# Optimization experiments

Measured on AMD Instinct MI355X. Metric: run time of the kernel, lower is better.

Reference implementation:

```python
import jax, jax.numpy as jnp
import numpy as np

B, S, D, H = 2, 2048, 1024, 16
HD = D // H  # head_dim = 64
SCALE = HD ** -0.5


def setup_inputs() -> dict:
    key = jax.random.key(0)
    k1, k2, k3 = jax.random.split(key, 3)
    src = jax.random.normal(k1, (B, S, D), dtype=jnp.float32)
    w_qkv = jax.random.normal(k2, (D, 3 * D), dtype=jnp.float32) * (D ** -0.5)
    b_qkv = jax.random.normal(k3, (3 * D,), dtype=jnp.float32) * 0.02
    return {"src": src, "w_qkv": w_qkv, "b_qkv": b_qkv}


def reference(src, w_qkv, b_qkv):
    # qkv projection: [B,S,3D]
    qkv = src @ w_qkv + b_qkv
    q, k, v = jnp.split(qkv, 3, axis=-1)
    # [B,S,D] -> [B,H,S,HD]
    def heads(x):
        return x.reshape(B, S, H, HD).transpose(0, 2, 1, 3)
    q, k, v = heads(q), heads(k), heads(v)
    # scaled dot-product attention (note: original scales AFTER q@k.T)
    attn = jnp.einsum('bhqd,bhkd->bhqk', q, k) * SCALE
    attn = jax.nn.softmax(attn, axis=-1)
    out = jnp.einsum('bhqk,bhkd->bhqd', attn, v)  # [B,H,S,HD]
    return out.transpose(0, 2, 1, 3).reshape(B, S, D)
```

## Files before the change

### kernel.cpp

```cpp
#include <hip/hip_runtime.h>
#include <hip/hip_bf16.h>

typedef short short8 __attribute__((ext_vector_type(8)));
typedef float f32x4 __attribute__((ext_vector_type(4)));
typedef float f32x16 __attribute__((ext_vector_type(16)));
typedef __hip_bfloat16 bf16;


__device__ __forceinline__ void glds16(const void* g, void* l) {
  __builtin_amdgcn_global_load_lds((const __attribute__((address_space(1))) unsigned int*)g,
                                   (__attribute__((address_space(3))) unsigned int*)l, 16, 0, 0);
}

__global__ __launch_bounds__(256) void cvt_src_kernel(const float4* __restrict__ in,
                                                      bf16* __restrict__ out, int n4) {
  int i = blockIdx.x * 256 + threadIdx.x;
  if (i >= n4) return;
  float4 v = in[i];
  union { bf16 h[4]; uint2 u; } pk;
  pk.h[0] = __float2bfloat16(v.x);
  pk.h[1] = __float2bfloat16(v.y);
  pk.h[2] = __float2bfloat16(v.z);
  pk.h[3] = __float2bfloat16(v.w);
  *(uint2*)(out + (size_t)i * 4) = pk.u;
}

__global__ __launch_bounds__(256) void transpose_w_kernel(const float* __restrict__ w,
                                                          bf16* __restrict__ wt) {
  __shared__ float tile[32][33];
  int x0 = blockIdx.x * 32;
  int y0 = blockIdx.y * 32;
  int tx = threadIdx.x & 31, ty = threadIdx.x >> 5;
#pragma unroll
  for (int i = 0; i < 4; i++) {
    int y = ty + i * 8;
    tile[y][tx] = w[(size_t)(y0 + y) * 3072 + x0 + tx];
  }
  __syncthreads();
#pragma unroll
  for (int i = 0; i < 4; i++) {
    int y = ty + i * 8;
    wt[(size_t)(x0 + y) * 1024 + y0 + tx] = __float2bfloat16(tile[tx][y]);
  }
}

__global__ __launch_bounds__(256) void qkv_gemm_kernel(
    const bf16* __restrict__ A, const bf16* __restrict__ Bt,
    const float* __restrict__ bias,
    bf16* __restrict__ q_ws, bf16* __restrict__ k_ws, bf16* __restrict__ vt_ws) {
  __shared__ alignas(16) char AB[32768];
  const int tid = threadIdx.x;
  const int lane = tid & 63, wid = tid >> 6;
  const int lr = lane & 15, lg = lane >> 4;
  const int wm = wid >> 1, wn = wid & 1;
  const int m0 = blockIdx.x * 128, n0 = blockIdx.y * 128;

  const f32x4 z4 = {0.f, 0.f, 0.f, 0.f};
  f32x4 acc[4][4];
#pragma unroll
  for (int m = 0; m < 4; m++)
#pragma unroll
    for (int n = 0; n < 4; n++) acc[m][n] = z4;

  const int srow = lane >> 3;
  const int sseg = (lane & 7) ^ srow;
  const char* Ag = (const char*)A + (size_t)(m0 + wid * 32 + srow) * 2048 + sseg * 16;
  const char* Bg = (const char*)Bt + (size_t)(n0 + wid * 32 + srow) * 2048 + sseg * 16;
  char* Al = AB + wid * 4096;
  char* Bl = AB + 16384 + wid * 4096;
  const int xora = (lr & 7) << 4;

  for (int kt = 0; kt < 16; kt++) {
    __syncthreads();
#pragma unroll
    for (int c = 0; c < 4; c++) {
      glds16(Ag + (size_t)kt * 128 + c * 16384, Al + c * 1024);
      glds16(Bg + (size_t)kt * 128 + c * 16384, Bl + c * 1024);
    }
    asm volatile("s_waitcnt vmcnt(0)" ::: "memory");
    __syncthreads();
#pragma unroll
    for (int g = 0; g < 2; g++) {
      short8 af[4], bfr[4];
#pragma unroll
      for (int m = 0; m < 4; m++)
        af[m] = *(const short8*)(AB + (wm * 64 + m * 16 + lr) * 128 +
                                 ((g * 64 + lg * 16) ^ xora));
#pragma unroll
      for (int n = 0; n < 4; n++)
        bfr[n] = *(const short8*)(AB + 16384 + (wn * 64 + n * 16 + lr) * 128 +
                                  ((g * 64 + lg * 16) ^ xora));
#pragma unroll
      for (int m = 0; m < 4; m++)
#pragma unroll
        for (int n = 0; n < 4; n++)
          acc[m][n] = __builtin_amdgcn_mfma_f32_16x16x32_bf16(af[m], bfr[n], acc[m][n], 0, 0, 0);
    }
  }

  const int which = n0 >> 10;
#pragma unroll
  for (int m = 0; m < 4; m++) {
    int row = m0 + wm * 64 + m * 16 + lg * 4;
    int b = row >> 11;
    int ss0 = row & 2047;
#pragma unroll
    for (int n = 0; n < 4; n++) {
      int col = n0 + wn * 64 + n * 16 + lr;
      int d = col & 1023;
      int h = d >> 6, hd = d & 63;
      size_t bh = (size_t)(b * 16 + h);
      float bv = bias[col];
      if (which == 2) {
        union { bf16 h4[4]; uint2 u; } pk;
#pragma unroll
        for (int r = 0; r < 4; r++) pk.h4[r] = __float2bfloat16(acc[m][n][r] + bv);
        *(uint2*)&vt_ws[(bh * 64 + hd) * 2048 + ss0] = pk.u;
      } else {
        bf16* dst = (which == 0) ? q_ws : k_ws;
#pragma unroll
        for (int r = 0; r < 4; r++)
          dst[(bh * 2048 + (ss0 + r)) * 64 + hd] = __float2bfloat16(acc[m][n][r] + bv);
      }
    }
  }
}

__global__ __launch_bounds__(512) void attn2_kernel(
    const bf16* __restrict__ q_ws, const bf16* __restrict__ k_ws,
    const bf16* __restrict__ vt_ws, float* __restrict__ out) {
  __shared__ alignas(16) char smem[65536];
  const int tid = threadIdx.x;
  const int lane = tid & 63, wid = tid >> 6;
  const int lq = lane & 31, hi = lane >> 5;
  const int hi16 = hi * 16;
  const int xorv = (lq & 7) << 4;
  const float scale_l2e = 0.125f * 1.44269504088896f;

  const int f = blockIdx.x;
  const int bh = (f & 7) * 4 + ((f >> 3) & 3);
  const int qb = f >> 5;
  const int b = bh >> 4, h = bh & 15;
  const int q0 = qb * 256 + wid * 32;

  short8 qf[4];
  {
    const bf16* qrow = q_ws + ((size_t)bh * 2048 + q0 + lq) * 64;
#pragma unroll
    for (int s = 0; s < 4; s++) qf[s] = *(const short8*)(qrow + s * 16 + hi * 8);
  }

  const int seg = (lane & 7) ^ (lane >> 3);
  const char* kgl = (const char*)k_ws + (size_t)bh * 2048 * 128 +
                    (size_t)(wid * 8 + (lane >> 3)) * 128 + seg * 16;
  const char* vgl = (const char*)vt_ws + (size_t)bh * 64 * 4096 +
                    (size_t)(wid * 8 + (lane >> 3)) * 4096 + seg * 16;

  f32x16 o0, o1;
#pragma unroll
  for (int r = 0; r < 16; r++) { o0[r] = 0.f; o1[r] = 0.f; }
  float m = -1e30f, l = 0.f;

#pragma unroll
  for (int p = 0; p < 3; p++) {
    glds16(kgl + (size_t)p * 8192, smem + p * 8192 + wid * 1024);
    glds16(vgl + (size_t)p * 128, smem + 32768 + p * 8192 + wid * 1024);
  }
  asm volatile("s_waitcnt vmcnt(4)" ::: "memory");
  __builtin_amdgcn_s_barrier();

  for (int kt = 0; kt < 32; ++kt) {
    const int buf = kt & 3;
    if (kt + 3 < 32) {
      glds16(kgl + (size_t)(kt + 3) * 8192, smem + ((kt + 3) & 3) * 8192 + wid * 1024);
      glds16(vgl + (size_t)(kt + 3) * 128, smem + 32768 + ((kt + 3) & 3) * 8192 + wid * 1024);
    }
    const int curK = buf * 8192;
    const int curV = 32768 + buf * 8192;

    f32x16 s0, s1;
#pragma unroll
    for (int r = 0; r < 16; r++) { s0[r] = 0.f; s1[r] = 0.f; }
#pragma unroll
    for (int s = 0; s < 4; s++) {
      const int doff = (s * 32 + hi16) ^ xorv;
      short8 k0 = *(const short8*)(smem + curK + lq * 128 + doff);
      short8 k1 = *(const short8*)(smem + curK + 4096 + lq * 128 + doff);
      __builtin_amdgcn_s_setprio(1);
      s0 = __builtin_amdgcn_mfma_f32_32x32x16_bf16(k0, qf[s], s0, 0, 0, 0);
      s1 = __builtin_amdgcn_mfma_f32_32x32x16_bf16(k1, qf[s], s1, 0, 0, 0);
      __builtin_amdgcn_s_setprio(0);
    }

    float mx[8];
#pragma unroll
    for (int r = 0; r < 16; r++) { s0[r] *= scale_l2e; s1[r] *= scale_l2e; }
#pragma unroll
    for (int i = 0; i < 8; i++) mx[i] = fmaxf(fmaxf(s0[i], s0[i + 8]), fmaxf(s1[i], s1[i + 8]));
#pragma unroll
    for (int i = 0; i < 4; i++) mx[i] = fmaxf(mx[i], mx[i + 4]);
    float pm = fmaxf(fmaxf(mx[0], mx[1]), fmaxf(mx[2], mx[3]));
    pm = fmaxf(pm, __shfl_xor(pm, 32));
    if (pm > m + 8.f) {
      float rs = __builtin_amdgcn_exp2f(m - pm);
      m = pm; l *= rs;
#pragma unroll
      for (int r = 0; r < 16; r++) { o0[r] *= rs; o1[r] *= rs; }
    }
    float sum[8];
#pragma unroll
    for (int r = 0; r < 16; r++) {
      s0[r] = __builtin_amdgcn_exp2f(s0[r] - m);
      s1[r] = __builtin_amdgcn_exp2f(s1[r] - m);
    }
#pragma unroll
    for (int i = 0; i < 8; i++) sum[i] = (s0[i] + s0[i + 8]) + (s1[i] + s1[i + 8]);
#pragma unroll
    for (int i = 0; i < 4; i++) sum[i] += sum[i + 4];
    float ps = (sum[0] + sum[1]) + (sum[2] + sum[3]);
    ps += __shfl_xor(ps, 32);
    l += ps;

#pragma unroll
    for (int kb = 0; kb < 2; kb++) {
      uint w[8], t[8];
#pragma unroll
      for (int i = 0; i < 8; i++) {
        union { bf16 h2[2]; uint u; } pk;
        float plo = kb ? s1[2 * i] : s0[2 * i];
        float phi = kb ? s1[2 * i + 1] : s0[2 * i + 1];
        pk.h2[0] = __float2bfloat16(plo);
        pk.h2[1] = __float2bfloat16(phi);
        w[i] = pk.u;
      }
#pragma unroll
      for (int i = 0; i < 8; i++) t[i] = (uint)__shfl_xor((int)w[i], 32);
      union { uint u[4]; short8 s; } ua, ub;
      ua.u[0] = hi ? t[2] : w[0];
      ua.u[1] = hi ? t[3] : w[1];
      ua.u[2] = hi ? w[2] : t[0];
      ua.u[3] = hi ? w[3] : t[1];
      ub.u[0] = hi ? t[6] : w[4];
      ub.u[1] = hi ? t[7] : w[5];
      ub.u[2] = hi ? w[6] : t[4];
      ub.u[3] = hi ? w[7] : t[5];
#pragma unroll
      for (int s = 0; s < 2; s++) {
        short8 pa = s ? ub.s : ua.s;
        const int koff = (kb * 64 + s * 32 + hi16) ^ xorv;
        short8 v0 = *(const short8*)(smem + curV + lq * 128 + koff);
        short8 v1 = *(const short8*)(smem + curV + 4096 + lq * 128 + koff);
        __builtin_amdgcn_s_setprio(1);
        o0 = __builtin_amdgcn_mfma_f32_32x32x16_bf16(v0, pa, o0, 0, 0, 0);
        o1 = __builtin_amdgcn_mfma_f32_32x32x16_bf16(v1, pa, o1, 0, 0, 0);
        __builtin_amdgcn_s_setprio(0);
      }
    }

    if (kt < 29)       asm volatile("s_waitcnt vmcnt(4)" ::: "memory");
    else if (kt == 29) asm volatile("s_waitcnt vmcnt(2)" ::: "memory");
    else if (kt == 30) asm volatile("s_waitcnt vmcnt(0)" ::: "memory");
    if (kt < 31) __builtin_amdgcn_s_barrier();
  }
  __syncthreads();

  float* ep = (float*)(smem) + wid * 1024;
  const float invl = 1.f / l;
  const int eq = lane >> 1, eds = lane & 1;
  float* obase = out + ((size_t)b * 2048 + qb * 256 + wid * 32 + eq) * 1024 +
                 h * 64 + eds * 16;
#pragma unroll
  for (int db = 0; db < 2; db++) {
#pragma unroll
    for (int r = 0; r < 16; r++) {
      int d = (r & 3) + 8 * (r >> 2) + 4 * hi;
      float v = (db ? o1[r] : o0[r]) * invl;
      ep[lq * 32 + ((d + lq) & 31)] = v;
    }
#pragma unroll
    for (int c = 0; c < 4; c++) {
      float4 t;
      t.x = ep[eq * 32 + ((eds * 16 + 4 * c + 0 + eq) & 31)];
      t.y = ep[eq * 32 + ((eds * 16 + 4 * c + 1 + eq) & 31)];
      t.z = ep[eq * 32 + ((eds * 16 + 4 * c + 2 + eq) & 31)];
      t.w = ep[eq * 32 + ((eds * 16 + 4 * c + 3 + eq) & 31)];
      *(float4*)(obase + db * 32 + 4 * c) = t;
    }
  }
}

extern "C" void kernel_launch(void* const* d_in, const int* in_sizes, int n_in,
                              void* d_out, int out_size, void* d_ws, size_t ws_size,
                              hipStream_t stream) {
  (void)in_sizes; (void)n_in; (void)out_size; (void)ws_size;
  const float* src  = (const float*)d_in[0];
  const float* w    = (const float*)d_in[1];
  const float* bias = (const float*)d_in[2];
  float* out = (float*)d_out;

  char* ws = (char*)d_ws;
  bf16* src_bf = (bf16*)ws;
  bf16* wt_bf  = (bf16*)(ws + 8388608);
  bf16* q_ws   = (bf16*)(ws + 8388608 + 6291456);
  bf16* k_ws   = q_ws + 4194304;
  bf16* vt_ws  = k_ws + 4194304;

  cvt_src_kernel<<<4096, 256, 0, stream>>>((const float4*)src, src_bf, 1048576);
  transpose_w_kernel<<<dim3(96, 32), 256, 0, stream>>>(w, wt_bf);
  qkv_gemm_kernel<<<dim3(32, 24), 256, 0, stream>>>(src_bf, wt_bf, bias, q_ws, k_ws, vt_ws);
  attn2_kernel<<<256, 512, 0, stream>>>(q_ws, k_ws, vt_ws, out);
}
```

Measured before the change: 107.7 us.

## Split attention KV range across two blocks and merge partials in new kernel

Attention grid doubles from 256 to 512 blocks. Each block processes half of the key/value sequence and writes an unnormalized partial output plus its running max and sum to workspace. A new merge kernel combines the two halves with log-sum-exp weights. The intent is to fill the MI355X's 256 CUs with more than one wave of blocks, at the cost of an extra launch and extra global traffic. The score scaling is also folded into an fma inside exp2, and the max is scaled once after reduction.

```diff
diff --git a/kernel.cpp b/kernel.cpp
--- a/kernel.cpp
+++ b/kernel.cpp
@@ -128,7 +128,7 @@
 
 __global__ __launch_bounds__(512) void attn2_kernel(
     const bf16* __restrict__ q_ws, const bf16* __restrict__ k_ws,
-    const bf16* __restrict__ vt_ws, float* __restrict__ out) {
+    const bf16* __restrict__ vt_ws, float* __restrict__ po, float* __restrict__ ml) {
   __shared__ alignas(16) char smem[65536];
   const int tid = threadIdx.x;
   const int lane = tid & 63, wid = tid >> 6;
@@ -138,9 +138,10 @@
   const float scale_l2e = 0.125f * 1.44269504088896f;
 
   const int f = blockIdx.x;
-  const int bh = (f & 7) * 4 + ((f >> 3) & 3);
-  const int qb = f >> 5;
-  const int b = bh >> 4, h = bh & 15;
+  const int ks = f & 1;
+  const int g = f >> 1;
+  const int bh = (g & 7) * 4 + ((g >> 3) & 3);
+  const int qb = g >> 5;
   const int q0 = qb * 256 + wid * 32;
 
   short8 qf[4];
@@ -151,9 +152,9 @@
   }
 
   const int seg = (lane & 7) ^ (lane >> 3);
-  const char* kgl = (const char*)k_ws + (size_t)bh * 2048 * 128 +
+  const char* kgl = (const char*)k_ws + (size_t)bh * 2048 * 128 + (size_t)ks * 16 * 8192 +
                     (size_t)(wid * 8 + (lane >> 3)) * 128 + seg * 16;
-  const char* vgl = (const char*)vt_ws + (size_t)bh * 64 * 4096 +
+  const char* vgl = (const char*)vt_ws + (size_t)bh * 64 * 4096 + ks * 2048 +
                     (size_t)(wid * 8 + (lane >> 3)) * 4096 + seg * 16;
 
   f32x16 o0, o1;
@@ -169,9 +170,9 @@
   asm volatile("s_waitcnt vmcnt(4)" ::: "memory");
   __builtin_amdgcn_s_barrier();
 
-  for (int kt = 0; kt < 32; ++kt) {
+  for (int kt = 0; kt < 16; ++kt) {
     const int buf = kt & 3;
-    if (kt + 3 < 32) {
+    if (kt + 3 < 16) {
       glds16(kgl + (size_t)(kt + 3) * 8192, smem + ((kt + 3) & 3) * 8192 + wid * 1024);
       glds16(vgl + (size_t)(kt + 3) * 128, smem + 32768 + ((kt + 3) & 3) * 8192 + wid * 1024);
     }
@@ -194,13 +195,12 @@
 
     float mx[8];
 #pragma unroll
-    for (int r = 0; r < 16; r++) { s0[r] *= scale_l2e; s1[r] *= scale_l2e; }
-#pragma unroll
     for (int i = 0; i < 8; i++) mx[i] = fmaxf(fmaxf(s0[i], s0[i + 8]), fmaxf(s1[i], s1[i + 8]));
 #pragma unroll
     for (int i = 0; i < 4; i++) mx[i] = fmaxf(mx[i], mx[i + 4]);
     float pm = fmaxf(fmaxf(mx[0], mx[1]), fmaxf(mx[2], mx[3]));
     pm = fmaxf(pm, __shfl_xor(pm, 32));
+    pm *= scale_l2e;
     if (pm > m + 8.f) {
       float rs = __builtin_amdgcn_exp2f(m - pm);
       m = pm; l *= rs;
@@ -210,8 +210,8 @@
     float sum[8];
 #pragma unroll
     for (int r = 0; r < 16; r++) {
-      s0[r] = __builtin_amdgcn_exp2f(s0[r] - m);
-      s1[r] = __builtin_amdgcn_exp2f(s1[r] - m);
+      s0[r] = __builtin_amdgcn_exp2f(__builtin_fmaf(s0[r], scale_l2e, -m));
+      s1[r] = __builtin_amdgcn_exp2f(__builtin_fmaf(s1[r], scale_l2e, -m));
     }
 #pragma unroll
     for (int i = 0; i < 8; i++) sum[i] = (s0[i] + s0[i + 8]) + (s1[i] + s1[i + 8]);
@@ -257,24 +257,26 @@
       }
     }
 
-    if (kt < 29)       asm volatile("s_waitcnt vmcnt(4)" ::: "memory");
-    else if (kt == 29) asm volatile("s_waitcnt vmcnt(2)" ::: "memory");
-    else if (kt == 30) asm volatile("s_waitcnt vmcnt(0)" ::: "memory");
-    if (kt < 31) __builtin_amdgcn_s_barrier();
+    if (kt < 13)       asm volatile("s_waitcnt vmcnt(4)" ::: "memory");
+    else if (kt == 13) asm volatile("s_waitcnt vmcnt(2)" ::: "memory");
+    else if (kt == 14) asm volatile("s_waitcnt vmcnt(0)" ::: "memory");
+    if (kt < 15) __builtin_amdgcn_s_barrier();
   }
   __syncthreads();
 
+  if (hi == 0) {
+    float2 v = {m, l};
+    *(float2*)&ml[((size_t)(ks * 32 + bh) * 2048 + q0 + lq) * 2] = v;
+  }
   float* ep = (float*)(smem) + wid * 1024;
-  const float invl = 1.f / l;
   const int eq = lane >> 1, eds = lane & 1;
-  float* obase = out + ((size_t)b * 2048 + qb * 256 + wid * 32 + eq) * 1024 +
-                 h * 64 + eds * 16;
+  float* pobase = po + ((size_t)(ks * 32 + bh) * 2048 + q0 + eq) * 64 + eds * 16;
 #pragma unroll
   for (int db = 0; db < 2; db++) {
 #pragma unroll
     for (int r = 0; r < 16; r++) {
       int d = (r & 3) + 8 * (r >> 2) + 4 * hi;
-      float v = (db ? o1[r] : o0[r]) * invl;
+      float v = (db ? o1[r] : o0[r]);
       ep[lq * 32 + ((d + lq) & 31)] = v;
     }
 #pragma unroll
@@ -284,9 +286,36 @@
       t.y = ep[eq * 32 + ((eds * 16 + 4 * c + 1 + eq) & 31)];
       t.z = ep[eq * 32 + ((eds * 16 + 4 * c + 2 + eq) & 31)];
       t.w = ep[eq * 32 + ((eds * 16 + 4 * c + 3 + eq) & 31)];
-      *(float4*)(obase + db * 32 + 4 * c) = t;
-    }
-  }
+      *(float4*)(pobase + db * 32 + 4 * c) = t;
+    }
+  }
+}
+
+__global__ __launch_bounds__(256) void merge_kernel(const float* __restrict__ po,
+                                                    const float* __restrict__ ml,
+                                                    float* __restrict__ out) {
+  int i = blockIdx.x * 256 + threadIdx.x;
+  int c4 = i & 255;
+  int bs = i >> 8;
+  int h = c4 >> 4, hd4 = c4 & 15;
+  int b = bs >> 11, s = bs & 2047;
+  size_t row0 = (size_t)(b * 16 + h) * 2048 + s;
+  size_t row1 = (size_t)(32 + b * 16 + h) * 2048 + s;
+  float2 ml0 = *(const float2*)&ml[row0 * 2];
+  float2 ml1 = *(const float2*)&ml[row1 * 2];
+  float M = fmaxf(ml0.x, ml1.x);
+  float w0 = __builtin_amdgcn_exp2f(ml0.x - M);
+  float w1 = __builtin_amdgcn_exp2f(ml1.x - M);
+  float inv = 1.f / (ml0.y * w0 + ml1.y * w1);
+  w0 *= inv; w1 *= inv;
+  float4 a = *(const float4*)&po[row0 * 64 + hd4 * 4];
+  float4 c = *(const float4*)&po[row1 * 64 + hd4 * 4];
+  float4 r;
+  r.x = a.x * w0 + c.x * w1;
+  r.y = a.y * w0 + c.y * w1;
+  r.z = a.z * w0 + c.z * w1;
+  r.w = a.w * w0 + c.w * w1;
+  *(float4*)&out[(size_t)bs * 1024 + c4 * 4] = r;
 }
 
 extern "C" void kernel_launch(void* const* d_in, const int* in_sizes, int n_in,
@@ -299,14 +328,17 @@
   float* out = (float*)d_out;
 
   char* ws = (char*)d_ws;
+  float* po = (float*)ws;
+  float* ml = (float*)(ws + 33554432);
   bf16* src_bf = (bf16*)ws;
   bf16* wt_bf  = (bf16*)(ws + 8388608);
-  bf16* q_ws   = (bf16*)(ws + 8388608 + 6291456);
+  bf16* q_ws   = (bf16*)(ws + 34603008);
   bf16* k_ws   = q_ws + 4194304;
   bf16* vt_ws  = k_ws + 4194304;
 
   cvt_src_kernel<<<4096, 256, 0, stream>>>((const float4*)src, src_bf, 1048576);
   transpose_w_kernel<<<dim3(96, 32), 256, 0, stream>>>(w, wt_bf);
   qkv_gemm_kernel<<<dim3(32, 24), 256, 0, stream>>>(src_bf, wt_bf, bias, q_ws, k_ws, vt_ws);
-  attn2_kernel<<<256, 512, 0, stream>>>(q_ws, k_ws, vt_ws, out);
-}
+  attn2_kernel<<<512, 512, 0, stream>>>(q_ws, k_ws, vt_ws, po, ml);
+  merge_kernel<<<4096, 256, 0, stream>>>(po, ml, out);
+}
```

After: 116.2 us. 7.9% more time.

## Process 128-key tiles with double buffering and split PV accumulators in attention

Applied to the files above, without the earlier changes.

The attention kernel now processes 128 keys per iteration instead of 64. It uses two shared-memory buffers in place of four, and a new swizzle layout for the V tile. That halves the number of barriers and waits, gives more independent MFMAs per tile, and uses two accumulator sets per output half so dependent MFMA chains are shorter. The scale is folded into an FMA inside exp2, and the lane-exchange shuffles are cut from 8 to 4 per key block. In exchange, register pressure rises and the prefetch is only one tile ahead, waiting on vmcnt(0) every iteration, which may expose load latency.

```diff
diff --git a/kernel.cpp b/kernel.cpp
--- a/kernel.cpp
+++ b/kernel.cpp
@@ -10,6 +10,13 @@
 __device__ __forceinline__ void glds16(const void* g, void* l) {
   __builtin_amdgcn_global_load_lds((const __attribute__((address_space(1))) unsigned int*)g,
                                    (__attribute__((address_space(3))) unsigned int*)l, 16, 0, 0);
+}
+
+__device__ __forceinline__ uint pk2(float a, float b) {
+  union { bf16 h2[2]; uint u; } pk;
+  pk.h2[0] = __float2bfloat16(a);
+  pk.h2[1] = __float2bfloat16(b);
+  return pk.u;
 }
 
 __global__ __launch_bounds__(256) void cvt_src_kernel(const float4* __restrict__ in,
@@ -126,7 +133,7 @@
   }
 }
 
-__global__ __launch_bounds__(512) void attn2_kernel(
+__global__ __launch_bounds__(512) void attn3_kernel(
     const bf16* __restrict__ q_ws, const bf16* __restrict__ k_ws,
     const bf16* __restrict__ vt_ws, float* __restrict__ out) {
   __shared__ alignas(16) char smem[65536];
@@ -150,120 +157,142 @@
     for (int s = 0; s < 4; s++) qf[s] = *(const short8*)(qrow + s * 16 + hi * 8);
   }
 
-  const int seg = (lane & 7) ^ (lane >> 3);
-  const char* kgl = (const char*)k_ws + (size_t)bh * 2048 * 128 +
-                    (size_t)(wid * 8 + (lane >> 3)) * 128 + seg * 16;
-  const char* vgl = (const char*)vt_ws + (size_t)bh * 64 * 4096 +
-                    (size_t)(wid * 8 + (lane >> 3)) * 4096 + seg * 16;
-
-  f32x16 o0, o1;
-#pragma unroll
-  for (int r = 0; r < 16; r++) { o0[r] = 0.f; o1[r] = 0.f; }
+  const int l8 = lane >> 3;
+  const int segk = (lane & 7) ^ l8;
+  const char* kgl = (const char*)k_ws + (size_t)bh * 262144 +
+                    (size_t)(wid * 16 + l8) * 128 + segk * 16;
+  const int l16 = lane >> 4;
+  const int d0v = (wid * 2 + 0) * 4 + l16;
+  const int d1v = (wid * 2 + 1) * 4 + l16;
+  const char* vg0 = (const char*)vt_ws + (size_t)bh * 262144 + (size_t)d0v * 4096 +
+                    (((lane & 15) ^ (d0v & 15)) << 4);
+  const char* vg1 = (const char*)vt_ws + (size_t)bh * 262144 + (size_t)d1v * 4096 +
+                    (((lane & 15) ^ (d1v & 15)) << 4);
+
+  f32x16 o0a, o0b, o1a, o1b;
+#pragma unroll
+  for (int r = 0; r < 16; r++) { o0a[r] = 0.f; o0b[r] = 0.f; o1a[r] = 0.f; o1b[r] = 0.f; }
   float m = -1e30f, l = 0.f;
 
-#pragma unroll
-  for (int p = 0; p < 3; p++) {
-    glds16(kgl + (size_t)p * 8192, smem + p * 8192 + wid * 1024);
-    glds16(vgl + (size_t)p * 128, smem + 32768 + p * 8192 + wid * 1024);
-  }
-  asm volatile("s_waitcnt vmcnt(4)" ::: "memory");
+  glds16(kgl, smem + wid * 2048);
+  glds16(kgl + 1024, smem + wid * 2048 + 1024);
+  glds16(vg0, smem + 32768 + wid * 2048);
+  glds16(vg1, smem + 32768 + wid * 2048 + 1024);
+  asm volatile("s_waitcnt vmcnt(0)" ::: "memory");
   __builtin_amdgcn_s_barrier();
 
-  for (int kt = 0; kt < 32; ++kt) {
-    const int buf = kt & 3;
-    if (kt + 3 < 32) {
-      glds16(kgl + (size_t)(kt + 3) * 8192, smem + ((kt + 3) & 3) * 8192 + wid * 1024);
-      glds16(vgl + (size_t)(kt + 3) * 128, smem + 32768 + ((kt + 3) & 3) * 8192 + wid * 1024);
-    }
-    const int curK = buf * 8192;
-    const int curV = 32768 + buf * 8192;
-
-    f32x16 s0, s1;
-#pragma unroll
-    for (int r = 0; r < 16; r++) { s0[r] = 0.f; s1[r] = 0.f; }
-#pragma unroll
-    for (int s = 0; s < 4; s++) {
-      const int doff = (s * 32 + hi16) ^ xorv;
-      short8 k0 = *(const short8*)(smem + curK + lq * 128 + doff);
-      short8 k1 = *(const short8*)(smem + curK + 4096 + lq * 128 + doff);
+  for (int kt = 0; kt < 16; ++kt) {
+    const int kb_off = (kt & 1) * 16384;
+    const int vb_off = 32768 + (kt & 1) * 16384;
+    if (kt + 1 < 16) {
+      const int nb = ((kt + 1) & 1) * 16384;
+      glds16(kgl + (size_t)(kt + 1) * 16384, smem + nb + wid * 2048);
+      glds16(kgl + (size_t)(kt + 1) * 16384 + 1024, smem + nb + wid * 2048 + 1024);
+      glds16(vg0 + (size_t)(kt + 1) * 256, smem + 32768 + nb + wid * 2048);
+      glds16(vg1 + (size_t)(kt + 1) * 256, smem + 32768 + nb + wid * 2048 + 1024);
+    }
+
+    f32x16 s0, s1, s2, s3;
+#pragma unroll
+    for (int r = 0; r < 16; r++) { s0[r] = 0.f; s1[r] = 0.f; s2[r] = 0.f; s3[r] = 0.f; }
+#pragma unroll
+    for (int st = 0; st < 4; st++) {
+      const int doff = (st * 32 + hi16) ^ xorv;
+      short8 ka = *(const short8*)(smem + kb_off + lq * 128 + doff);
+      short8 kb = *(const short8*)(smem + kb_off + (lq + 32) * 128 + doff);
+      short8 kc = *(const short8*)(smem + kb_off + (lq + 64) * 128 + doff);
+      short8 kd = *(const short8*)(smem + kb_off + (lq + 96) * 128 + doff);
       __builtin_amdgcn_s_setprio(1);
-      s0 = __builtin_amdgcn_mfma_f32_32x32x16_bf16(k0, qf[s], s0, 0, 0, 0);
-      s1 = __builtin_amdgcn_mfma_f32_32x32x16_bf16(k1, qf[s], s1, 0, 0, 0);
+      s0 = __builtin_amdgcn_mfma_f32_32x32x16_bf16(ka, qf[st], s0, 0, 0, 0);
+      s1 = __builtin_amdgcn_mfma_f32_32x32x16_bf16(kb, qf[st], s1, 0, 0, 0);
+      s2 = __builtin_amdgcn_mfma_f32_32x32x16_bf16(kc, qf[st], s2, 0, 0, 0);
+      s3 = __builtin_amdgcn_mfma_f32_32x32x16_bf16(kd, qf[st], s3, 0, 0, 0);
       __builtin_amdgcn_s_setprio(0);
     }
 
-    float mx[8];
-#pragma unroll
-    for (int r = 0; r < 16; r++) { s0[r] *= scale_l2e; s1[r] *= scale_l2e; }
-#pragma unroll
-    for (int i = 0; i < 8; i++) mx[i] = fmaxf(fmaxf(s0[i], s0[i + 8]), fmaxf(s1[i], s1[i + 8]));
+    float mx[16];
+#pragma unroll
+    for (int i = 0; i < 16; i++)
+      mx[i] = fmaxf(fmaxf(s0[i], s1[i]), fmaxf(s2[i], s3[i]));
+#pragma unroll
+    for (int i = 0; i < 8; i++) mx[i] = fmaxf(mx[i], mx[i + 8]);
 #pragma unroll
     for (int i = 0; i < 4; i++) mx[i] = fmaxf(mx[i], mx[i + 4]);
     float pm = fmaxf(fmaxf(mx[0], mx[1]), fmaxf(mx[2], mx[3]));
     pm = fmaxf(pm, __shfl_xor(pm, 32));
+    pm *= scale_l2e;
     if (pm > m + 8.f) {
       float rs = __builtin_amdgcn_exp2f(m - pm);
       m = pm; l *= rs;
 #pragma unroll
-      for (int r = 0; r < 16; r++) { o0[r] *= rs; o1[r] *= rs; }
-    }
-    float sum[8];
+      for (int r = 0; r < 16; r++) {
+        o0a[r] *= rs; o0b[r] *= rs; o1a[r] *= rs; o1b[r] *= rs;
+      }
+    }
 #pragma unroll
     for (int r = 0; r < 16; r++) {
-      s0[r] = __builtin_amdgcn_exp2f(s0[r] - m);
-      s1[r] = __builtin_amdgcn_exp2f(s1[r] - m);
-    }
-#pragma unroll
-    for (int i = 0; i < 8; i++) sum[i] = (s0[i] + s0[i + 8]) + (s1[i] + s1[i + 8]);
-#pragma unroll
-    for (int i = 0; i < 4; i++) sum[i] += sum[i + 4];
-    float ps = (sum[0] + sum[1]) + (sum[2] + sum[3]);
-    ps += __shfl_xor(ps, 32);
-    l += ps;
-
-#pragma unroll
-    for (int kb = 0; kb < 2; kb++) {
-      uint w[8], t[8];
-#pragma unroll
-      for (int i = 0; i < 8; i++) {
-        union { bf16 h2[2]; uint u; } pk;
-        float plo = kb ? s1[2 * i] : s0[2 * i];
-        float phi = kb ? s1[2 * i + 1] : s0[2 * i + 1];
-        pk.h2[0] = __float2bfloat16(plo);
-        pk.h2[1] = __float2bfloat16(phi);
-        w[i] = pk.u;
-      }
-#pragma unroll
-      for (int i = 0; i < 8; i++) t[i] = (uint)__shfl_xor((int)w[i], 32);
-      union { uint u[4]; short8 s; } ua, ub;
-      ua.u[0] = hi ? t[2] : w[0];
-      ua.u[1] = hi ? t[3] : w[1];
-      ua.u[2] = hi ? w[2] : t[0];
-      ua.u[3] = hi ? w[3] : t[1];
-      ub.u[0] = hi ? t[6] : w[4];
-      ub.u[1] = hi ? t[7] : w[5];
-      ub.u[2] = hi ? w[6] : t[4];
-      ub.u[3] = hi ? w[7] : t[5];
-#pragma unroll
-      for (int s = 0; s < 2; s++) {
-        short8 pa = s ? ub.s : ua.s;
-        const int koff = (kb * 64 + s * 32 + hi16) ^ xorv;
-        short8 v0 = *(const short8*)(smem + curV + lq * 128 + koff);
-        short8 v1 = *(const short8*)(smem + curV + 4096 + lq * 128 + koff);
-        __builtin_amdgcn_s_setprio(1);
-        o0 = __builtin_amdgcn_mfma_f32_32x32x16_bf16(v0, pa, o0, 0, 0, 0);
-        o1 = __builtin_amdgcn_mfma_f32_32x32x16_bf16(v1, pa, o1, 0, 0, 0);
-        __builtin_amdgcn_s_setprio(0);
-      }
-    }
-
-    if (kt < 29)       asm volatile("s_waitcnt vmcnt(4)" ::: "memory");
-    else if (kt == 29) asm volatile("s_waitcnt vmcnt(2)" ::: "memory");
-    else if (kt == 30) asm volatile("s_waitcnt vmcnt(0)" ::: "memory");
-    if (kt < 31) __builtin_amdgcn_s_barrier();
+      s0[r] = __builtin_amdgcn_exp2f(__builtin_fmaf(s0[r], scale_l2e, -m));
+      s1[r] = __builtin_amdgcn_exp2f(__builtin_fmaf(s1[r], scale_l2e, -m));
+      s2[r] = __builtin_amdgcn_exp2f(__builtin_fmaf(s2[r], scale_l2e, -m));
+      s3[r] = __builtin_amdgcn_exp2f(__builtin_fmaf(s3[r], scale_l2e, -m));
+    }
+    {
+      float sm[16];
+#pragma unroll
+      for (int i = 0; i < 16; i++) sm[i] = (s0[i] + s1[i]) + (s2[i] + s3[i]);
+#pragma unroll
+      for (int i = 0; i < 8; i++) sm[i] += sm[i + 8];
+#pragma unroll
+      for (int i = 0; i < 4; i++) sm[i] += sm[i + 4];
+      float ps = (sm[0] + sm[1]) + (sm[2] + sm[3]);
+      ps += __shfl_xor(ps, 32);
+      l += ps;
+    }
+
+#define PV_KB(S, KB, OA, OB)                                                     \
+  {                                                                              \
+    uint w0 = pk2(S[0], S[1]), w1 = pk2(S[2], S[3]);                             \
+    uint w2 = pk2(S[4], S[5]), w3 = pk2(S[6], S[7]);                             \
+    uint w4 = pk2(S[8], S[9]), w5 = pk2(S[10], S[11]);                           \
+    uint w6 = pk2(S[12], S[13]), w7 = pk2(S[14], S[15]);                         \
+    uint r0 = (uint)__shfl_xor((int)(hi ? w0 : w2), 32);                         \
+    uint r1 = (uint)__shfl_xor((int)(hi ? w1 : w3), 32);                         \
+    uint r2 = (uint)__shfl_xor((int)(hi ? w4 : w6), 32);                         \
+    uint r3 = (uint)__shfl_xor((int)(hi ? w5 : w7), 32);                         \
+    union { uint u[4]; short8 s8; } ua, ub;                                      \
+    ua.u[0] = hi ? r0 : w0; ua.u[1] = hi ? r1 : w1;                              \
+    ua.u[2] = hi ? w2 : r0; ua.u[3] = hi ? w3 : r1;                              \
+    ub.u[0] = hi ? r2 : w4; ub.u[1] = hi ? r3 : w5;                              \
+    ub.u[2] = hi ? w6 : r2; ub.u[3] = hi ? w7 : r3;                              \
+    const int c0 = (((KB) * 4 + hi) ^ (lq & 15)) << 4;                           \
+    const int c1 = (((KB) * 4 + 2 + hi) ^ (lq & 15)) << 4;                       \
+    short8 va0 = *(const short8*)(smem + vb_off + lq * 256 + c0);                \
+    short8 va1 = *(const short8*)(smem + vb_off + (lq + 32) * 256 + c0);         \
+    short8 vb0 = *(const short8*)(smem + vb_off + lq * 256 + c1);                \
+    short8 vb1 = *(const short8*)(smem + vb_off + (lq + 32) * 256 + c1);         \
+    __builtin_amdgcn_s_setprio(1);                                               \
+    OA = __builtin_amdgcn_mfma_f32_32x32x16_bf16(va0, ua.s8, OA, 0, 0, 0);       \
+    OB = __builtin_amdgcn_mfma_f32_32x32x16_bf16(va1, ua.s8, OB, 0, 0, 0);       \
+    OA = __builtin_amdgcn_mfma_f32_32x32x16_bf16(vb0, ub.s8, OA, 0, 0, 0);       \
+    OB = __builtin_amdgcn_mfma_f32_32x32x16_bf16(vb1, ub.s8, OB, 0, 0, 0);       \
+    __builtin_amdgcn_s_setprio(0);                                               \
+  }
+    PV_KB(s0, 0, o0a, o1a)
+    PV_KB(s1, 1, o0b, o1b)
+    PV_KB(s2, 2, o0a, o1a)
+    PV_KB(s3, 3, o0b, o1b)
+#undef PV_KB
+
+    if (kt < 15) {
+      asm volatile("s_waitcnt vmcnt(0)" ::: "memory");
+      __builtin_amdgcn_s_barrier();
+    }
   }
   __syncthreads();
 
+  f32x16 o0, o1;
+#pragma unroll
+  for (int r = 0; r < 16; r++) { o0[r] = o0a[r] + o0b[r]; o1[r] = o1a[r] + o1b[r]; }
   float* ep = (float*)(smem) + wid * 1024;
   const float invl = 1.f / l;
   const int eq = lane >> 1, eds = lane & 1;
@@ -308,5 +337,5 @@
   cvt_src_kernel<<<4096, 256, 0, stream>>>((const float4*)src, src_bf, 1048576);
   transpose_w_kernel<<<dim3(96, 32), 256, 0, stream>>>(w, wt_bf);
   qkv_gemm_kernel<<<dim3(32, 24), 256, 0, stream>>>(src_bf, wt_bf, bias, q_ws, k_ws, vt_ws);
-  attn2_kernel<<<256, 512, 0, stream>>>(q_ws, k_ws, vt_ws, out);
-}
+  attn3_kernel<<<256, 512, 0, stream>>>(q_ws, k_ws, vt_ws, out);
+}
```

Result: faster. 102.7 us (-4.6%).
